# Kernel optimization log

Measured on AMD Instinct MI355X. Metric: run time of the kernel, lower is better.

The kernel has to match this reference:

```python
import jax, jax.numpy as jnp
import numpy as np

IO, LAT, HID, NV = 64, 32, 60, 16

def setup_inputs() -> dict:
    key = jax.random.key(0)
    ks = jax.random.split(key, 11)
    def lin(k, fan_out, fan_in):
        kw, kb = jax.random.split(k)
        bound = 1.0 / np.sqrt(fan_in)
        w = jax.random.uniform(kw, (fan_out, fan_in), jnp.float32, -bound, bound)
        b = jax.random.uniform(kb, (fan_out,), jnp.float32, -bound, bound)
        return w, b
    enc1_w, enc1_b = lin(ks[0], HID, IO)
    mean_w, mean_b = lin(ks[1], LAT, HID)
    std_w, std_b = lin(ks[2], LAT, HID)
    dec1_w, dec1_b = lin(ks[3], HID, LAT)
    dec2_w, dec2_b = lin(ks[4], IO, HID)
    h_input = jax.random.normal(ks[5], (4096, 16, IO), jnp.float32)
    return {"h_input": h_input, "num_traj": 8,
            "enc1_w": enc1_w, "enc1_b": enc1_b, "mean_w": mean_w, "mean_b": mean_b,
            "std_w": std_w, "std_b": std_b, "dec1_w": dec1_w, "dec1_b": dec1_b,
            "dec2_w": dec2_w, "dec2_b": dec2_b}

def reference(h_input, num_traj, enc1_w, enc1_b, mean_w, mean_b, std_w, std_b, dec1_w, dec1_b, dec2_w, dec2_b):
    B, H, _ = h_input.shape
    x = h_input.reshape(-1, IO)               # [N, io]
    N = x.shape[0]
    h1 = jax.nn.relu(x @ enc1_w.T + enc1_b)   # [N, 60]
    mu = h1 @ mean_w.T + mean_b               # [N, L]
    logvar = h1 @ std_w.T + std_b             # [N, L]
    std = jnp.exp(0.5 * logvar)
    eps = jax.random.normal(jax.random.key(1), (num_traj, N, LAT), jnp.float32)
    z = mu[None] + eps * std[None]            # [T, N, L]
    # on-device closed-form standard-normal pdf (replaces scipy host roundtrip)
    log_pdf = -0.5 * (LAT * jnp.log(2.0 * jnp.pi) + jnp.sum(eps * eps, axis=-1))  # [T, N]
    pdf = jnp.exp(log_pdf)
    # decode, batched over trajectories
    h3 = jax.nn.relu(jnp.einsum('tnl,hl->tnh', z, dec1_w) + dec1_b)
    out = jnp.einsum('tnh,oh->tno', h3, dec2_w) + dec2_b          # [T, N, io]
    traj = out.reshape(num_traj, N, H, IO // H).transpose(0, 2, 1, 3)  # [T, H, N, io/H]
    p = jnp.exp(pdf)                          # faithful: exp of the pdf values
    p = p / jnp.sum(p, axis=0)                # normalize over trajectories
    prob_list = p.reshape(num_traj, -1, NV)   # [T, N/NV, NV]
    return traj, mu, logvar, prob_list
```

## Files before the change

kernel.cpp:

```cpp
#include <hip/hip_runtime.h>
#include <cstdint>


#define TPB_A 256
#define NBLK_A 256
#define TPB_B 256
#define NBLK_B 2048

__device__ __forceinline__ void threefry2x32_01(uint32_t c0, uint32_t c1,
                                                uint32_t& o0, uint32_t& o1) {
  uint32_t x0 = c0;
  uint32_t x1 = c1 + 1u;
#define TFR(r) { x0 += x1; x1 = (x1 << (r)) | (x1 >> (32 - (r))); x1 ^= x0; }
  TFR(13) TFR(15) TFR(26) TFR(6)
  x0 += 1u;          x1 += 0x1BD11BDCu;
  TFR(17) TFR(29) TFR(16) TFR(24)
  x0 += 0x1BD11BDBu; x1 += 2u;
  TFR(13) TFR(15) TFR(26) TFR(6)
        x1 += 4u;
  TFR(17) TFR(29) TFR(16) TFR(24)
  x0 += 1u;          x1 += 0x1BD11BDFu;
  TFR(13) TFR(15) TFR(26) TFR(6)
  x0 += 0x1BD11BDBu; x1 += 5u;
#undef TFR
  o0 = x0; o1 = x1;
}

__device__ __forceinline__ uint32_t threefry_bits_partitionable(uint32_t idx) {
  uint32_t o0, o1;
  threefry2x32_01(0u, idx, o0, o1);
  return o0 ^ o1;
}

__device__ __forceinline__ float bits_to_normal(uint32_t b) {
  const float lo = -0.99999994f;
  float f = __uint_as_float((b >> 9) | 0x3F800000u) - 1.0f;
  float u = fmaxf(f * 2.0f + lo, lo);
  return 1.41421356f * erfinvf(u);
}

__global__ __launch_bounds__(TPB_A, 1) void vae_encode(
    const float* __restrict__ X,
    const float* __restrict__ w1, const float* __restrict__ b1,
    const float* __restrict__ wm, const float* __restrict__ bm,
    const float* __restrict__ wsd, const float* __restrict__ bsd,
    float* __restrict__ out) {
  const int tid = threadIdx.x;
  const int n = blockIdx.x * TPB_A + tid;

  float x[64];
  {
    const float4* xr = (const float4*)(X + (size_t)n * 64);
#pragma unroll
    for (int q = 0; q < 16; ++q) {
      float4 v = xr[q];
      x[4 * q + 0] = v.x; x[4 * q + 1] = v.y;
      x[4 * q + 2] = v.z; x[4 * q + 3] = v.w;
    }
  }

  float mu[32], lv[32];
#pragma unroll
  for (int i = 0; i < 32; ++i) { mu[i] = bm[i]; lv[i] = bsd[i]; }
  for (int j = 0; j < 60; ++j) {
    const float4* wr = (const float4*)(w1 + j * 64);
    float a0 = 0.f, a1 = 0.f, a2 = 0.f, a3 = 0.f;
#pragma unroll
    for (int q = 0; q < 16; ++q) {
      float4 w = wr[q];
      a0 = fmaf(w.x, x[4 * q + 0], a0);
      a1 = fmaf(w.y, x[4 * q + 1], a1);
      a2 = fmaf(w.z, x[4 * q + 2], a2);
      a3 = fmaf(w.w, x[4 * q + 3], a3);
    }
    float h = fmaxf((a0 + a1) + (a2 + a3) + b1[j], 0.f);
    const float* wmc = wm + j;
    const float* wsc = wsd + j;
#pragma unroll
    for (int i = 0; i < 32; ++i) {
      mu[i] = fmaf(wmc[i * 60], h, mu[i]);
      lv[i] = fmaf(wsc[i * 60], h, lv[i]);
    }
  }

  float4* muo = (float4*)(out + (size_t)33554432 + (size_t)n * 32);
  float4* lvo = (float4*)(out + (size_t)35651584 + (size_t)n * 32);
#pragma unroll
  for (int g = 0; g < 8; ++g) {
    float4 v; v.x = mu[4 * g + 0]; v.y = mu[4 * g + 1];
    v.z = mu[4 * g + 2]; v.w = mu[4 * g + 3];
    muo[g] = v;
    float4 w; w.x = lv[4 * g + 0]; w.y = lv[4 * g + 1];
    w.z = lv[4 * g + 2]; w.w = lv[4 * g + 3];
    lvo[g] = w;
  }
}

__global__ __launch_bounds__(TPB_B, 4) void vae_decode(
    const float* __restrict__ wd1, const float* __restrict__ bd1,
    const float* __restrict__ wd2, const float* __restrict__ bd2,
    float* __restrict__ out) {
  const int tid = threadIdx.x;
  const int g = blockIdx.x * TPB_B + tid;
  const int n = g & 65535;
  const int t = g >> 16;

  const float4* mur = (const float4*)(out + (size_t)33554432 + (size_t)n * 32);
  const float4* lvr = (const float4*)(out + (size_t)35651584 + (size_t)n * 32);
  const uint32_t cbase = (uint32_t)t * 2097152u + (uint32_t)n * 32u;
  float z[32];
#pragma unroll
  for (int gq = 0; gq < 8; ++gq) {
    float4 m4 = mur[gq];
    float4 v4 = lvr[gq];
    float s0 = expf(0.5f * v4.x), s1 = expf(0.5f * v4.y);
    float s2 = expf(0.5f * v4.z), s3 = expf(0.5f * v4.w);
    uint32_t c = cbase + (uint32_t)(4 * gq);
    z[4 * gq + 0] = fmaf(bits_to_normal(threefry_bits_partitionable(c + 0u)), s0, m4.x);
    z[4 * gq + 1] = fmaf(bits_to_normal(threefry_bits_partitionable(c + 1u)), s1, m4.y);
    z[4 * gq + 2] = fmaf(bits_to_normal(threefry_bits_partitionable(c + 2u)), s2, m4.z);
    z[4 * gq + 3] = fmaf(bits_to_normal(threefry_bits_partitionable(c + 3u)), s3, m4.w);
  }

  float h3[60];
#pragma unroll
  for (int j = 0; j < 60; ++j) {
    const float* wj = wd1 + j * 32;
    float a = bd1[j];
#pragma unroll
    for (int l = 0; l < 32; ++l) a = fmaf(wj[l], z[l], a);
    h3[j] = fmaxf(a, 0.f);
  }

  {
    float4* trj = (float4*)out + (size_t)(t * 16) * 65536 + n;
    const float4* bd24 = (const float4*)bd2;
    for (int hh = 0; hh < 16; ++hh) {
      const float4* w0 = (const float4*)(wd2 + (hh * 4 + 0) * 60);
      const float4* w1r = (const float4*)(wd2 + (hh * 4 + 1) * 60);
      const float4* w2 = (const float4*)(wd2 + (hh * 4 + 2) * 60);
      const float4* w3 = (const float4*)(wd2 + (hh * 4 + 3) * 60);
      float a0 = 0.f, a1 = 0.f, a2 = 0.f, a3 = 0.f;
#pragma unroll
      for (int q = 0; q < 15; ++q) {
        float4 wa = w0[q], wb = w1r[q], wc = w2[q], wdv = w3[q];
        float h0 = h3[4 * q + 0], hv1 = h3[4 * q + 1];
        float hv2 = h3[4 * q + 2], hv3 = h3[4 * q + 3];
        a0 = fmaf(wa.x, h0, a0); a0 = fmaf(wa.y, hv1, a0);
        a0 = fmaf(wa.z, hv2, a0); a0 = fmaf(wa.w, hv3, a0);
        a1 = fmaf(wb.x, h0, a1); a1 = fmaf(wb.y, hv1, a1);
        a1 = fmaf(wb.z, hv2, a1); a1 = fmaf(wb.w, hv3, a1);
        a2 = fmaf(wc.x, h0, a2); a2 = fmaf(wc.y, hv1, a2);
        a2 = fmaf(wc.z, hv2, a2); a2 = fmaf(wc.w, hv3, a2);
        a3 = fmaf(wdv.x, h0, a3); a3 = fmaf(wdv.y, hv1, a3);
        a3 = fmaf(wdv.z, hv2, a3); a3 = fmaf(wdv.w, hv3, a3);
      }
      float4 bb = bd24[hh];
      float4 o;
      o.x = a0 + bb.x; o.y = a1 + bb.y; o.z = a2 + bb.z; o.w = a3 + bb.w;
      trj[(size_t)hh * 65536] = o;
    }
  }

  out[(size_t)37748736 + (size_t)t * 65536 + (size_t)n] = 0.125f;
}

extern "C" void kernel_launch(void* const* d_in, const int* in_sizes, int n_in,
                              void* d_out, int out_size, void* d_ws, size_t ws_size,
                              hipStream_t stream) {
  const float* X   = (const float*)d_in[0];
  const float* w1  = (const float*)d_in[2];
  const float* b1  = (const float*)d_in[3];
  const float* wm  = (const float*)d_in[4];
  const float* bm  = (const float*)d_in[5];
  const float* wsd = (const float*)d_in[6];
  const float* bsd = (const float*)d_in[7];
  const float* wd1 = (const float*)d_in[8];
  const float* bd1 = (const float*)d_in[9];
  const float* wd2 = (const float*)d_in[10];
  const float* bd2 = (const float*)d_in[11];

  vae_encode<<<NBLK_A, TPB_A, 0, stream>>>(X, w1, b1, wm, bm, wsd, bsd,
                                           (float*)d_out);
  vae_decode<<<NBLK_B, TPB_B, 0, stream>>>(wd1, bd1, wd2, bd2, (float*)d_out);
}
```

Baseline: 407.7 us.

## Split encoder output columns across four waves to raise encode parallelism

The encoder now gives each 64-row tile to a 256-thread block in which each of the four waves computes 8 of the 32 mu/logvar outputs, instead of one thread computing all 32 for its row. The block count rises from 256 to 1024 and the launch bound allows four blocks per CU. This is meant to improve latency hiding and occupancy in the encode stage and to cut per-thread register use. In exchange, every wave recomputes the full 60-wide hidden layer, so that part of the arithmetic is done four times.

```diff
diff --git a/kernel.cpp b/kernel.cpp
--- a/kernel.cpp
+++ b/kernel.cpp
@@ -3,7 +3,7 @@
 
 
 #define TPB_A 256
-#define NBLK_A 256
+#define NBLK_A 1024
 #define TPB_B 256
 #define NBLK_B 2048
 
@@ -39,14 +39,17 @@
   return 1.41421356f * erfinvf(u);
 }
 
-__global__ __launch_bounds__(TPB_A, 1) void vae_encode(
+__global__ __launch_bounds__(TPB_A, 4) void vae_encode(
     const float* __restrict__ X,
     const float* __restrict__ w1, const float* __restrict__ b1,
     const float* __restrict__ wm, const float* __restrict__ bm,
     const float* __restrict__ wsd, const float* __restrict__ bsd,
     float* __restrict__ out) {
   const int tid = threadIdx.x;
-  const int n = blockIdx.x * TPB_A + tid;
+  const int lane = tid & 63;
+  const int slot = __builtin_amdgcn_readfirstlane(tid >> 6);
+  const int i0 = slot * 8;
+  const int n = blockIdx.x * 64 + lane;
 
   float x[64];
   {
@@ -59,9 +62,9 @@
     }
   }
 
-  float mu[32], lv[32];
+  float mu[8], lv[8];
 #pragma unroll
-  for (int i = 0; i < 32; ++i) { mu[i] = bm[i]; lv[i] = bsd[i]; }
+  for (int ii = 0; ii < 8; ++ii) { mu[ii] = bm[i0 + ii]; lv[ii] = bsd[i0 + ii]; }
   for (int j = 0; j < 60; ++j) {
     const float4* wr = (const float4*)(w1 + j * 64);
     float a0 = 0.f, a1 = 0.f, a2 = 0.f, a3 = 0.f;
@@ -74,26 +77,24 @@
       a3 = fmaf(w.w, x[4 * q + 3], a3);
     }
     float h = fmaxf((a0 + a1) + (a2 + a3) + b1[j], 0.f);
-    const float* wmc = wm + j;
-    const float* wsc = wsd + j;
+    const float* wmc = wm + i0 * 60 + j;
+    const float* wsc = wsd + i0 * 60 + j;
 #pragma unroll
-    for (int i = 0; i < 32; ++i) {
-      mu[i] = fmaf(wmc[i * 60], h, mu[i]);
-      lv[i] = fmaf(wsc[i * 60], h, lv[i]);
+    for (int ii = 0; ii < 8; ++ii) {
+      mu[ii] = fmaf(wmc[ii * 60], h, mu[ii]);
+      lv[ii] = fmaf(wsc[ii * 60], h, lv[ii]);
     }
   }
 
-  float4* muo = (float4*)(out + (size_t)33554432 + (size_t)n * 32);
-  float4* lvo = (float4*)(out + (size_t)35651584 + (size_t)n * 32);
-#pragma unroll
-  for (int g = 0; g < 8; ++g) {
-    float4 v; v.x = mu[4 * g + 0]; v.y = mu[4 * g + 1];
-    v.z = mu[4 * g + 2]; v.w = mu[4 * g + 3];
-    muo[g] = v;
-    float4 w; w.x = lv[4 * g + 0]; w.y = lv[4 * g + 1];
-    w.z = lv[4 * g + 2]; w.w = lv[4 * g + 3];
-    lvo[g] = w;
-  }
+  float4* muo = (float4*)(out + (size_t)33554432 + (size_t)n * 32 + i0);
+  float4* lvo = (float4*)(out + (size_t)35651584 + (size_t)n * 32 + i0);
+  float4 v0, v1, w0, w1v;
+  v0.x = mu[0]; v0.y = mu[1]; v0.z = mu[2]; v0.w = mu[3];
+  v1.x = mu[4]; v1.y = mu[5]; v1.z = mu[6]; v1.w = mu[7];
+  w0.x = lv[0]; w0.y = lv[1]; w0.z = lv[2]; w0.w = lv[3];
+  w1v.x = lv[4]; w1v.y = lv[5]; w1v.z = lv[6]; w1v.w = lv[7];
+  muo[0] = v0; muo[1] = v1;
+  lvo[0] = w0; lvo[1] = w1v;
 }
 
 __global__ __launch_bounds__(TPB_B, 4) void vae_decode(
```

Measured after the change: 388.0 us. -4.8%, faster.
